# Performance work log

Hardware: AMD Instinct MI355X
Metric: run time of the kernel (lower is better)

Reference implementation:

```python
import jax, jax.numpy as jnp
import numpy as np

INPUT_SIZE = 1024
HIDDEN = 2048
B = 4096


def setup_inputs() -> dict:
    key = jax.random.key(0)
    ks = jax.random.split(key, 11)
    D = INPUT_SIZE + HIDDEN
    bound = 1.0 / np.sqrt(D)  # nn.Linear default init range
    def lin(kw, kb):
        W = jax.random.uniform(kw, (HIDDEN, D), jnp.float32, -bound, bound)
        b = jax.random.uniform(kb, (HIDDEN,), jnp.float32, -bound, bound)
        return W, b
    W_i, b_i = lin(ks[0], ks[1])
    W_f, b_f = lin(ks[2], ks[3])
    W_c, b_c = lin(ks[4], ks[5])
    W_o, b_o = lin(ks[6], ks[7])
    x_t = jax.random.normal(ks[8], (B, INPUT_SIZE), jnp.float32)
    h_prev = jax.random.normal(ks[9], (B, HIDDEN), jnp.float32)
    c_prev = jax.random.normal(ks[10], (B, HIDDEN), jnp.float32)
    return {
        "x_t": x_t, "h_prev": h_prev, "c_prev": c_prev,
        "W_i": W_i, "b_i": b_i, "W_f": W_f, "b_f": b_f,
        "W_c": W_c, "b_c": b_c, "W_o": W_o, "b_o": b_o,
    }


def reference(x_t, h_prev, c_prev, W_i, b_i, W_f, b_f, W_c, b_c, W_o, b_o):
    # combined: [B, input+hidden]
    combined = jnp.concatenate([x_t, h_prev], axis=1)
    # fused gate GEMM: stack the four weight matrices -> one [D, 4H] matmul
    W_all = jnp.concatenate([W_i, W_f, W_c, W_o], axis=0)  # [4H, D]
    b_all = jnp.concatenate([b_i, b_f, b_c, b_o], axis=0)  # [4H]
    gates = combined @ W_all.T + b_all                     # [B, 4H]
    gi, gf, gc, go = jnp.split(gates, 4, axis=1)
    i_t = jax.nn.sigmoid(gi)
    f_t = jax.nn.sigmoid(gf)
    g_t = jnp.tanh(gc)
    o_t = jax.nn.sigmoid(go)
    c_t = f_t * c_prev + i_t * g_t
    h_t = o_t * jnp.tanh(c_t)
    # dropout is identity in eval / p=0
    return (h_t, c_t)
```

## Files before the change

kernel.cpp:

```cpp
#include <hip/hip_runtime.h>
#include <stdint.h>

#define B_DIM 4096
#define IN_SZ 1024
#define HID   2048
#define D_DIM 3072
#define BM 256
#define BN 64
#define BK 64
#define NT (D_DIM / BK)

typedef float  f32x4  __attribute__((ext_vector_type(4)));
typedef short  short8 __attribute__((ext_vector_type(8)));

__device__ __forceinline__ unsigned short f2bf(float f) {
    union { float f; unsigned u; } v; v.f = f;
    unsigned u = v.u + 0x7fffu + ((v.u >> 16) & 1u);
    return (unsigned short)(u >> 16);
}

__device__ __forceinline__ void async_load16(const void* g, void* l) {
    __builtin_amdgcn_global_load_lds(
        (const __attribute__((address_space(1))) unsigned int*)g,
        (__attribute__((address_space(3))) unsigned int*)l,
        16, 0, 0);
}

__device__ __forceinline__ float sigm(float x) {
    return 1.0f / (1.0f + __expf(-x));
}
__device__ __forceinline__ float tanh_f(float x) {
    return 1.0f - 2.0f / (__expf(2.0f * x) + 1.0f);
}

__global__ __launch_bounds__(256)
void convert_all(const float* __restrict__ x, const float* __restrict__ h,
                 const float* __restrict__ W0, const float* __restrict__ W1,
                 const float* __restrict__ W2, const float* __restrict__ W3,
                 unsigned short* __restrict__ Abf, unsigned short* __restrict__ Wbf) {
    const int NA = B_DIM * D_DIM / 8;
    const int NW = 4 * HID * D_DIM / 8;
    int idx = blockIdx.x * blockDim.x + threadIdx.x;
    const float* src;
    unsigned short* dst;
    if (idx < NA) {
        const int C8 = D_DIM / 8;
        int b = idx / C8, c8 = idx - b * C8;
        src = (c8 < IN_SZ / 8) ? x + (size_t)b * IN_SZ + c8 * 8
                               : h + (size_t)b * HID + (c8 - IN_SZ / 8) * 8;
        dst = Abf + (size_t)idx * 8;
    } else {
        int wi = idx - NA;
        if (wi >= NW) return;
        const int PG = HID * D_DIM / 8;
        int g = wi / PG, r = wi - g * PG;
        const float* W = (g == 0) ? W0 : (g == 1) ? W1 : (g == 2) ? W2 : W3;
        src = W + (size_t)r * 8;
        dst = Wbf + (size_t)wi * 8;
    }
    float4 v0 = ((const float4*)src)[0];
    float4 v1 = ((const float4*)src)[1];
    short8 o;
    o[0] = (short)f2bf(v0.x); o[1] = (short)f2bf(v0.y);
    o[2] = (short)f2bf(v0.z); o[3] = (short)f2bf(v0.w);
    o[4] = (short)f2bf(v1.x); o[5] = (short)f2bf(v1.y);
    o[6] = (short)f2bf(v1.z); o[7] = (short)f2bf(v1.w);
    *(short8*)dst = o;
}

template <int IB>
__device__ __forceinline__ void mfma16(f32x4 (&acc)[8][4], const short8 (&a)[4],
                                       const short8 (&b)[4]) {
#pragma unroll
    for (int i = 0; i < 4; ++i)
#pragma unroll
        for (int j = 0; j < 4; ++j)
            acc[IB + i][j] = __builtin_amdgcn_mfma_f32_16x16x32_bf16(
                a[i], b[j], acc[IB + i][j], 0, 0, 0);
}

template <int MODE>
__device__ __forceinline__ void tile_body(
    f32x4 (&acc)[8][4], const char* cur, char* nxt,
    const unsigned short* srcA0, const unsigned short* const* srcB,
    int koff, int chunk, int aBase, int bBase, int sw0, int sw1) {
    const char* curA = cur;
    const char* curB = cur + 32768;
    short8 a0s0[4], a1s0[4], a0s1[4], a1s1[4], bs0[4], bs1[4];

#pragma unroll
    for (int i = 0; i < 4; ++i)
        a0s0[i] = *(const short8*)(curA + aBase + i * 2048 + sw0);
#pragma unroll
    for (int j = 0; j < 4; ++j)
        bs0[j] = *(const short8*)(curB + bBase + j * 2048 + sw0);
#pragma unroll
    for (int i = 0; i < 4; ++i)
        a1s0[i] = *(const short8*)(curA + aBase + (4 + i) * 2048 + sw0);
    if (MODE) {
#pragma unroll
        for (int i = 0; i < 4; ++i)
            async_load16(srcA0 + i * 8 * D_DIM + koff, nxt + chunk + i * 1024);
    }
    __builtin_amdgcn_sched_barrier(0);
    __builtin_amdgcn_s_setprio(1);
    mfma16<0>(acc, a0s0, bs0);
    __builtin_amdgcn_s_setprio(0);

#pragma unroll
    for (int i = 0; i < 4; ++i)
        a0s1[i] = *(const short8*)(curA + aBase + i * 2048 + sw1);
#pragma unroll
    for (int j = 0; j < 4; ++j)
        bs1[j] = *(const short8*)(curB + bBase + j * 2048 + sw1);
    if (MODE) {
#pragma unroll
        for (int i = 0; i < 4; ++i)
            async_load16(srcB[i] + koff, nxt + 32768 + chunk + i * 1024);
    }
    __builtin_amdgcn_sched_barrier(0);
    __builtin_amdgcn_s_setprio(1);
    mfma16<4>(acc, a1s0, bs0);
    __builtin_amdgcn_s_setprio(0);

#pragma unroll
    for (int i = 0; i < 4; ++i)
        a1s1[i] = *(const short8*)(curA + aBase + (4 + i) * 2048 + sw1);
    __builtin_amdgcn_sched_barrier(0);
    __builtin_amdgcn_s_setprio(1);
    mfma16<0>(acc, a0s1, bs1);
    __builtin_amdgcn_s_setprio(0);

    __builtin_amdgcn_sched_barrier(0);
    __builtin_amdgcn_s_setprio(1);
    mfma16<4>(acc, a1s1, bs1);
    __builtin_amdgcn_s_setprio(0);
    if (MODE) {
        asm volatile("s_waitcnt vmcnt(0)" ::: "memory");
        __builtin_amdgcn_s_barrier();
        asm volatile("" ::: "memory");
    }
}

__global__ __launch_bounds__(512, 2)
void lstm_gemm(const unsigned short* __restrict__ Abf,
               const unsigned short* __restrict__ Wbf,
               const float* __restrict__ b_i, const float* __restrict__ b_f,
               const float* __restrict__ b_c, const float* __restrict__ b_o,
               const float* __restrict__ c_prev,
               float* __restrict__ h_out, float* __restrict__ c_out) {
    extern __shared__ char sm[];

    const int tid  = threadIdx.x;
    const int lane = tid & 63;
    const int wave = tid >> 6;
    const int wm   = wave >> 2;
    const int wn   = wave & 3;
    const int l16  = lane & 15;
    const int quad = lane >> 4;
    const int r7   = l16 & 7;

    const int m0 = blockIdx.x * BM;
    const int h0 = blockIdx.y * BN;

    const int g8 = lane >> 3;
    const int sl = (lane & 7) ^ g8;
    const unsigned short* srcA0 = Abf + (size_t)(m0 + wave * 32 + g8) * D_DIM + sl * 8;
    const unsigned short* srcB[4];
#pragma unroll
    for (int i = 0; i < 4; ++i) {
        const int rt = wave * 32 + i * 8 + g8;
        const int grow = ((rt >> 4) & 3) * HID + h0 + (rt >> 6) * 16 + (rt & 15);
        srcB[i] = Wbf + (size_t)grow * D_DIM + sl * 8;
    }
    const int chunk = wave * 4096;

    const int aBase = (wm * 128 + l16) * 128;
    const int bBase = (wn * 64  + l16) * 128;
    const int sw0 = ((0 * 4 + quad) ^ r7) * 16;
    const int sw1 = ((1 * 4 + quad) ^ r7) * 16;

    f32x4 acc[8][4] = {};

#pragma unroll
    for (int i = 0; i < 4; ++i) {
        async_load16(srcB[i], sm + 32768 + chunk + i * 1024);
        async_load16(srcA0 + i * 8 * D_DIM, sm + chunk + i * 1024);
    }
    asm volatile("s_waitcnt vmcnt(0)" ::: "memory");
    __builtin_amdgcn_s_barrier();
    asm volatile("" ::: "memory");

    for (int kt = 0; kt < NT - 1; ++kt) {
        const char* cur = sm + (kt & 1) * 65536;
        char* nxt = (char*)sm + ((kt + 1) & 1) * 65536;
        tile_body<1>(acc, cur, nxt, srcA0, srcB,
                     (kt + 1) * BK, chunk, aBase, bBase, sw0, sw1);
    }
    tile_body<0>(acc, sm + ((NT - 1) & 1) * 65536, (char*)sm,
                 srcA0, srcB, 0, chunk, aBase, bBase, sw0, sw1);

    const int h = h0 + wn * 16 + l16;
    const float biv = b_i[h], bfv = b_f[h], bcv = b_c[h], bov = b_o[h];
    const int mb = m0 + wm * 128 + quad * 4;
#pragma unroll
    for (int i = 0; i < 8; ++i) {
#pragma unroll
        for (int r = 0; r < 4; ++r) {
            const int m = mb + i * 16 + r;
            const size_t off = (size_t)m * HID + h;
            const float gi = acc[i][0][r] + biv;
            const float gf = acc[i][1][r] + bfv;
            const float gc = acc[i][2][r] + bcv;
            const float go = acc[i][3][r] + bov;
            const float it = sigm(gi), ft = sigm(gf);
            const float gt = tanh_f(gc), ot = sigm(go);
            const float c = ft * c_prev[off] + it * gt;
            h_out[off] = ot * tanh_f(c);
            c_out[off] = c;
        }
    }
}

extern "C" void kernel_launch(void* const* d_in, const int* in_sizes, int n_in,
                              void* d_out, int out_size, void* d_ws, size_t ws_size,
                              hipStream_t stream) {
    const float* x_t    = (const float*)d_in[0];
    const float* h_prev = (const float*)d_in[1];
    const float* c_prev = (const float*)d_in[2];
    const float* W_i = (const float*)d_in[3];
    const float* b_i = (const float*)d_in[4];
    const float* W_f = (const float*)d_in[5];
    const float* b_f = (const float*)d_in[6];
    const float* W_c = (const float*)d_in[7];
    const float* b_c = (const float*)d_in[8];
    const float* W_o = (const float*)d_in[9];
    const float* b_o = (const float*)d_in[10];
    float* out = (float*)d_out;

    unsigned short* Abf = (unsigned short*)d_ws;
    unsigned short* Wbf = (unsigned short*)((char*)d_ws + (size_t)B_DIM * D_DIM * 2);

    static bool s_attr = false;
    if (!s_attr) {
        (void)hipFuncSetAttribute((const void*)lstm_gemm,
                                  hipFuncAttributeMaxDynamicSharedMemorySize, 131072);
        s_attr = true;
    }

    {
        const int n = (B_DIM * D_DIM + 4 * HID * D_DIM) / 8;
        convert_all<<<n / 256, 256, 0, stream>>>(x_t, h_prev, W_i, W_f, W_c, W_o,
                                                 Abf, Wbf);
    }
    dim3 grid(B_DIM / BM, HID / BN);
    lstm_gemm<<<grid, 512, 131072, stream>>>(Abf, Wbf, b_i, b_f, b_c, b_o, c_prev,
                                             out, out + (size_t)B_DIM * HID);
}
```

Measured before the change: 383.7 us.

## Prepack weights in MFMA fragment order and load B directly into registers

```diff
diff --git a/kernel.cpp b/kernel.cpp
--- a/kernel.cpp
+++ b/kernel.cpp
@@ -52,10 +52,18 @@
     } else {
         int wi = idx - NA;
         if (wi >= NW) return;
-        const int PG = HID * D_DIM / 8;
-        int g = wi / PG, r = wi - g * PG;
-        const float* W = (g == 0) ? W0 : (g == 1) ? W1 : (g == 2) ? W2 : W3;
-        src = W + (size_t)r * 8;
+        int l  = wi & 63;
+        int q  = wi >> 6;
+        int s  = q & 1;
+        int j  = (q >> 1) & 3;
+        int wn = (q >> 3) & 3;
+        int q3 = q >> 5;
+        int kt = q3 % NT;
+        int c  = q3 / NT;
+        const float* W = (j == 0) ? W0 : (j == 1) ? W1 : (j == 2) ? W2 : W3;
+        int hrow = c * 64 + wn * 16 + (l & 15);
+        int k    = kt * 64 + s * 32 + (l >> 4) * 8;
+        src = W + (size_t)hrow * D_DIM + k;
         dst = Wbf + (size_t)wi * 8;
     }
     float4 v0 = ((const float4*)src)[0];
@@ -68,72 +76,66 @@
     *(short8*)dst = o;
 }
 
-template <int IB>
+template <int IB, int S>
 __device__ __forceinline__ void mfma16(f32x4 (&acc)[8][4], const short8 (&a)[4],
-                                       const short8 (&b)[4]) {
+                                       const short8 (&b)[4][2]) {
 #pragma unroll
     for (int i = 0; i < 4; ++i)
 #pragma unroll
         for (int j = 0; j < 4; ++j)
             acc[IB + i][j] = __builtin_amdgcn_mfma_f32_16x16x32_bf16(
-                a[i], b[j], acc[IB + i][j], 0, 0, 0);
+                a[i], b[j][S], acc[IB + i][j], 0, 0, 0);
 }
 
 template <int MODE>
 __device__ __forceinline__ void tile_body(
-    f32x4 (&acc)[8][4], const char* cur, char* nxt,
-    const unsigned short* srcA0, const unsigned short* const* srcB,
-    int koff, int chunk, int aBase, int bBase, int sw0, int sw1) {
-    const char* curA = cur;
-    const char* curB = cur + 32768;
-    short8 a0s0[4], a1s0[4], a0s1[4], a1s1[4], bs0[4], bs1[4];
-
-#pragma unroll
-    for (int i = 0; i < 4; ++i)
-        a0s0[i] = *(const short8*)(curA + aBase + i * 2048 + sw0);
-#pragma unroll
-    for (int j = 0; j < 4; ++j)
-        bs0[j] = *(const short8*)(curB + bBase + j * 2048 + sw0);
-#pragma unroll
-    for (int i = 0; i < 4; ++i)
-        a1s0[i] = *(const short8*)(curA + aBase + (4 + i) * 2048 + sw0);
+    f32x4 (&acc)[8][4], const short8 (&bc)[4][2], short8 (&bn)[4][2],
+    const char* cur, char* nxt,
+    const unsigned short* pBn,
+    const unsigned short* srcA0,
+    int koff, int chunk, int aBase, int sw0, int sw1) {
+    short8 f1[4], f2[4], f3[4], f4[4];
+
+#pragma unroll
+    for (int i = 0; i < 4; ++i)
+        f1[i] = *(const short8*)(cur + aBase + i * 2048 + sw0);
+#pragma unroll
+    for (int i = 0; i < 4; ++i)
+        f2[i] = *(const short8*)(cur + aBase + (4 + i) * 2048 + sw0);
     if (MODE) {
+#pragma unroll
+        for (int j = 0; j < 4; ++j) {
+            bn[j][0] = *(const short8*)(pBn + (j * 2 + 0) * 512);
+            bn[j][1] = *(const short8*)(pBn + (j * 2 + 1) * 512);
+        }
 #pragma unroll
         for (int i = 0; i < 4; ++i)
             async_load16(srcA0 + i * 8 * D_DIM + koff, nxt + chunk + i * 1024);
     }
     __builtin_amdgcn_sched_barrier(0);
     __builtin_amdgcn_s_setprio(1);
-    mfma16<0>(acc, a0s0, bs0);
-    __builtin_amdgcn_s_setprio(0);
-
-#pragma unroll
-    for (int i = 0; i < 4; ++i)
-        a0s1[i] = *(const short8*)(curA + aBase + i * 2048 + sw1);
-#pragma unroll
-    for (int j = 0; j < 4; ++j)
-        bs1[j] = *(const short8*)(curB + bBase + j * 2048 + sw1);
-    if (MODE) {
-#pragma unroll
-        for (int i = 0; i < 4; ++i)
-            async_load16(srcB[i] + koff, nxt + 32768 + chunk + i * 1024);
-    }
-    __builtin_amdgcn_sched_barrier(0);
-    __builtin_amdgcn_s_setprio(1);
-    mfma16<4>(acc, a1s0, bs0);
-    __builtin_amdgcn_s_setprio(0);
-
-#pragma unroll
-    for (int i = 0; i < 4; ++i)
-        a1s1[i] = *(const short8*)(curA + aBase + (4 + i) * 2048 + sw1);
-    __builtin_amdgcn_sched_barrier(0);
-    __builtin_amdgcn_s_setprio(1);
-    mfma16<0>(acc, a0s1, bs1);
-    __builtin_amdgcn_s_setprio(0);
-
-    __builtin_amdgcn_sched_barrier(0);
-    __builtin_amdgcn_s_setprio(1);
-    mfma16<4>(acc, a1s1, bs1);
+    mfma16<0, 0>(acc, f1, bc);
+    __builtin_amdgcn_s_setprio(0);
+
+#pragma unroll
+    for (int i = 0; i < 4; ++i)
+        f3[i] = *(const short8*)(cur + aBase + i * 2048 + sw1);
+    __builtin_amdgcn_sched_barrier(0);
+    __builtin_amdgcn_s_setprio(1);
+    mfma16<4, 0>(acc, f2, bc);
+    __builtin_amdgcn_s_setprio(0);
+
+#pragma unroll
+    for (int i = 0; i < 4; ++i)
+        f4[i] = *(const short8*)(cur + aBase + (4 + i) * 2048 + sw1);
+    __builtin_amdgcn_sched_barrier(0);
+    __builtin_amdgcn_s_setprio(1);
+    mfma16<0, 1>(acc, f3, bc);
+    __builtin_amdgcn_s_setprio(0);
+
+    __builtin_amdgcn_sched_barrier(0);
+    __builtin_amdgcn_s_setprio(1);
+    mfma16<4, 1>(acc, f4, bc);
     __builtin_amdgcn_s_setprio(0);
     if (MODE) {
         asm volatile("s_waitcnt vmcnt(0)" ::: "memory");
@@ -160,45 +162,57 @@
     const int quad = lane >> 4;
     const int r7   = l16 & 7;
 
-    const int m0 = blockIdx.x * BM;
-    const int h0 = blockIdx.y * BN;
+    const int hwid = blockIdx.x;
+    const int c    = (hwid & 7) + 8 * ((hwid >> 3) & 3);
+    const int bx   = hwid >> 5;
+    const int m0 = bx * BM;
+    const int h0 = c * BN;
 
     const int g8 = lane >> 3;
     const int sl = (lane & 7) ^ g8;
     const unsigned short* srcA0 = Abf + (size_t)(m0 + wave * 32 + g8) * D_DIM + sl * 8;
-    const unsigned short* srcB[4];
-#pragma unroll
-    for (int i = 0; i < 4; ++i) {
-        const int rt = wave * 32 + i * 8 + g8;
-        const int grow = ((rt >> 4) & 3) * HID + h0 + (rt >> 6) * 16 + (rt & 15);
-        srcB[i] = Wbf + (size_t)grow * D_DIM + sl * 8;
-    }
     const int chunk = wave * 4096;
 
+    const unsigned short* pB = Wbf + ((size_t)(c * NT) * 4 + wn) * 4096 + lane * 8;
+
     const int aBase = (wm * 128 + l16) * 128;
-    const int bBase = (wn * 64  + l16) * 128;
     const int sw0 = ((0 * 4 + quad) ^ r7) * 16;
     const int sw1 = ((1 * 4 + quad) ^ r7) * 16;
 
     f32x4 acc[8][4] = {};
-
-#pragma unroll
-    for (int i = 0; i < 4; ++i) {
-        async_load16(srcB[i], sm + 32768 + chunk + i * 1024);
+    short8 b0[4][2], b1[4][2];
+
+#pragma unroll
+    for (int j = 0; j < 4; ++j) {
+        b0[j][0] = *(const short8*)(pB + (j * 2 + 0) * 512);
+        b0[j][1] = *(const short8*)(pB + (j * 2 + 1) * 512);
+    }
+#pragma unroll
+    for (int i = 0; i < 4; ++i)
         async_load16(srcA0 + i * 8 * D_DIM, sm + chunk + i * 1024);
-    }
     asm volatile("s_waitcnt vmcnt(0)" ::: "memory");
     __builtin_amdgcn_s_barrier();
     asm volatile("" ::: "memory");
-
-    for (int kt = 0; kt < NT - 1; ++kt) {
-        const char* cur = sm + (kt & 1) * 65536;
-        char* nxt = (char*)sm + ((kt + 1) & 1) * 65536;
-        tile_body<1>(acc, cur, nxt, srcA0, srcB,
-                     (kt + 1) * BK, chunk, aBase, bBase, sw0, sw1);
-    }
-    tile_body<0>(acc, sm + ((NT - 1) & 1) * 65536, (char*)sm,
-                 srcA0, srcB, 0, chunk, aBase, bBase, sw0, sw1);
+    pB += 16384;
+
+    for (int kt = 0; kt < NT - 2; kt += 2) {
+        const char* e = sm + (kt & 1) * 32768;
+        char*       o = (char*)sm + ((kt + 1) & 1) * 32768;
+        tile_body<1>(acc, b0, b1, e, o, pB, srcA0, (kt + 1) * BK,
+                     chunk, aBase, sw0, sw1);
+        pB += 16384;
+        tile_body<1>(acc, b1, b0, o, (char*)e, pB, srcA0, (kt + 2) * BK,
+                     chunk, aBase, sw0, sw1);
+        pB += 16384;
+    }
+    {
+        tile_body<1>(acc, b0, b1, sm, (char*)sm + 32768, pB, srcA0,
+                     (NT - 1) * BK, chunk, aBase, sw0, sw1);
+    }
+    {
+        tile_body<0>(acc, b1, b0, sm + 32768, (char*)sm, pB, srcA0,
+                     0, chunk, aBase, sw0, sw1);
+    }
 
     const int h = h0 + wn * 16 + l16;
     const float biv = b_i[h], bfv = b_f[h], bcv = b_c[h], bov = b_o[h];
@@ -215,9 +229,9 @@
             const float go = acc[i][3][r] + bov;
             const float it = sigm(gi), ft = sigm(gf);
             const float gt = tanh_f(gc), ot = sigm(go);
-            const float c = ft * c_prev[off] + it * gt;
-            h_out[off] = ot * tanh_f(c);
-            c_out[off] = c;
+            const float cc = ft * c_prev[off] + it * gt;
+            h_out[off] = ot * tanh_f(cc);
+            c_out[off] = cc;
         }
     }
 }
@@ -244,7 +258,7 @@
     static bool s_attr = false;
     if (!s_attr) {
         (void)hipFuncSetAttribute((const void*)lstm_gemm,
-                                  hipFuncAttributeMaxDynamicSharedMemorySize, 131072);
+                                  hipFuncAttributeMaxDynamicSharedMemorySize, 65536);
         s_attr = true;
     }
 
@@ -253,7 +267,6 @@
         convert_all<<<n / 256, 256, 0, stream>>>(x_t, h_prev, W_i, W_f, W_c, W_o,
                                                  Abf, Wbf);
     }
-    dim3 grid(B_DIM / BM, HID / BN);
-    lstm_gemm<<<grid, 512, 131072, stream>>>(Abf, Wbf, b_i, b_f, b_c, b_o, c_prev,
-                                             out, out + (size_t)B_DIM * HID);
-}
+    lstm_gemm<<<512, 512, 65536, stream>>>(Abf, Wbf, b_i, b_f, b_c, b_o, c_prev,
+                                           out, out + (size_t)B_DIM * HID);
+}
```

Measured after the change: 389.9 us. No clear change (+1.6%).

## Use four-stage LDS ring of 32-wide K slices with deeper async prefetch

Applied to the files above, without the earlier changes.

```diff
diff --git a/kernel.cpp b/kernel.cpp
--- a/kernel.cpp
+++ b/kernel.cpp
@@ -7,8 +7,8 @@
 #define D_DIM 3072
 #define BM 256
 #define BN 64
-#define BK 64
-#define NT (D_DIM / BK)
+#define BK2 128
+#define NT2 (D_DIM / BK2)
 
 typedef float  f32x4  __attribute__((ext_vector_type(4)));
 typedef short  short8 __attribute__((ext_vector_type(8)));
@@ -40,32 +40,34 @@
                  unsigned short* __restrict__ Abf, unsigned short* __restrict__ Wbf) {
     const int NA = B_DIM * D_DIM / 8;
     const int NW = 4 * HID * D_DIM / 8;
-    int idx = blockIdx.x * blockDim.x + threadIdx.x;
-    const float* src;
-    unsigned short* dst;
-    if (idx < NA) {
-        const int C8 = D_DIM / 8;
-        int b = idx / C8, c8 = idx - b * C8;
-        src = (c8 < IN_SZ / 8) ? x + (size_t)b * IN_SZ + c8 * 8
-                               : h + (size_t)b * HID + (c8 - IN_SZ / 8) * 8;
-        dst = Abf + (size_t)idx * 8;
-    } else {
-        int wi = idx - NA;
-        if (wi >= NW) return;
-        const int PG = HID * D_DIM / 8;
-        int g = wi / PG, r = wi - g * PG;
-        const float* W = (g == 0) ? W0 : (g == 1) ? W1 : (g == 2) ? W2 : W3;
-        src = W + (size_t)r * 8;
-        dst = Wbf + (size_t)wi * 8;
-    }
-    float4 v0 = ((const float4*)src)[0];
-    float4 v1 = ((const float4*)src)[1];
-    short8 o;
-    o[0] = (short)f2bf(v0.x); o[1] = (short)f2bf(v0.y);
-    o[2] = (short)f2bf(v0.z); o[3] = (short)f2bf(v0.w);
-    o[4] = (short)f2bf(v1.x); o[5] = (short)f2bf(v1.y);
-    o[6] = (short)f2bf(v1.z); o[7] = (short)f2bf(v1.w);
-    *(short8*)dst = o;
+    const int total = NA + NW;
+    for (int idx = blockIdx.x * blockDim.x + threadIdx.x; idx < total;
+         idx += gridDim.x * blockDim.x) {
+        const float* src;
+        unsigned short* dst;
+        if (idx < NA) {
+            const int C8 = D_DIM / 8;
+            int b = idx / C8, c8 = idx - b * C8;
+            src = (c8 < IN_SZ / 8) ? x + (size_t)b * IN_SZ + c8 * 8
+                                   : h + (size_t)b * HID + (c8 - IN_SZ / 8) * 8;
+            dst = Abf + (size_t)idx * 8;
+        } else {
+            int wi = idx - NA;
+            const int PG = HID * D_DIM / 8;
+            int g = wi / PG, r = wi - g * PG;
+            const float* W = (g == 0) ? W0 : (g == 1) ? W1 : (g == 2) ? W2 : W3;
+            src = W + (size_t)r * 8;
+            dst = Wbf + (size_t)wi * 8;
+        }
+        float4 v0 = ((const float4*)src)[0];
+        float4 v1 = ((const float4*)src)[1];
+        short8 o;
+        o[0] = (short)f2bf(v0.x); o[1] = (short)f2bf(v0.y);
+        o[2] = (short)f2bf(v0.z); o[3] = (short)f2bf(v0.w);
+        o[4] = (short)f2bf(v1.x); o[5] = (short)f2bf(v1.y);
+        o[6] = (short)f2bf(v1.z); o[7] = (short)f2bf(v1.w);
+        *(short8*)dst = o;
+    }
 }
 
 template <int IB>
@@ -79,67 +81,36 @@
                 a[i], b[j], acc[IB + i][j], 0, 0, 0);
 }
 
-template <int MODE>
-__device__ __forceinline__ void tile_body(
-    f32x4 (&acc)[8][4], const char* cur, char* nxt,
-    const unsigned short* srcA0, const unsigned short* const* srcB,
-    int koff, int chunk, int aBase, int bBase, int sw0, int sw1) {
-    const char* curA = cur;
-    const char* curB = cur + 32768;
-    short8 a0s0[4], a1s0[4], a0s1[4], a1s1[4], bs0[4], bs1[4];
-
+template <int KS, int SKS>
+__device__ __forceinline__ void pair_body(
+    f32x4 (&acc)[8][4], char* sm, int aOff, int bOff, int wchunk,
+    const unsigned short* sA, const unsigned short* sB0, const unsigned short* sB1,
+    int stElem) {
+    const char* reg = sm + KS * 16384;
+    short8 a0[4], bb[4], a1[4];
 #pragma unroll
     for (int i = 0; i < 4; ++i)
-        a0s0[i] = *(const short8*)(curA + aBase + i * 2048 + sw0);
+        a0[i] = *(const short8*)(reg + aOff + i * 1024);
 #pragma unroll
     for (int j = 0; j < 4; ++j)
-        bs0[j] = *(const short8*)(curB + bBase + j * 2048 + sw0);
+        bb[j] = *(const short8*)(reg + bOff + j * 1024);
 #pragma unroll
     for (int i = 0; i < 4; ++i)
-        a1s0[i] = *(const short8*)(curA + aBase + (4 + i) * 2048 + sw0);
-    if (MODE) {
-#pragma unroll
-        for (int i = 0; i < 4; ++i)
-            async_load16(srcA0 + i * 8 * D_DIM + koff, nxt + chunk + i * 1024);
-    }
+        a1[i] = *(const short8*)(reg + aOff + (4 + i) * 1024);
+    char* dA = sm + SKS * 16384 + wchunk;
+    char* dB = dA + 65536;
+    async_load16(sA + stElem,         dA);
+    async_load16(sA + 49152 + stElem, dA + 1024);
+    async_load16(sB0 + stElem,        dB);
+    async_load16(sB1 + stElem,        dB + 1024);
     __builtin_amdgcn_sched_barrier(0);
     __builtin_amdgcn_s_setprio(1);
-    mfma16<0>(acc, a0s0, bs0);
+    mfma16<0>(acc, a0, bb);
+    mfma16<4>(acc, a1, bb);
     __builtin_amdgcn_s_setprio(0);
-
-#pragma unroll
-    for (int i = 0; i < 4; ++i)
-        a0s1[i] = *(const short8*)(curA + aBase + i * 2048 + sw1);
-#pragma unroll
-    for (int j = 0; j < 4; ++j)
-        bs1[j] = *(const short8*)(curB + bBase + j * 2048 + sw1);
-    if (MODE) {
-#pragma unroll
-        for (int i = 0; i < 4; ++i)
-            async_load16(srcB[i] + koff, nxt + 32768 + chunk + i * 1024);
-    }
-    __builtin_amdgcn_sched_barrier(0);
-    __builtin_amdgcn_s_setprio(1);
-    mfma16<4>(acc, a1s0, bs0);
-    __builtin_amdgcn_s_setprio(0);
-
-#pragma unroll
-    for (int i = 0; i < 4; ++i)
-        a1s1[i] = *(const short8*)(curA + aBase + (4 + i) * 2048 + sw1);
-    __builtin_amdgcn_sched_barrier(0);
-    __builtin_amdgcn_s_setprio(1);
-    mfma16<0>(acc, a0s1, bs1);
-    __builtin_amdgcn_s_setprio(0);
-
-    __builtin_amdgcn_sched_barrier(0);
-    __builtin_amdgcn_s_setprio(1);
-    mfma16<4>(acc, a1s1, bs1);
-    __builtin_amdgcn_s_setprio(0);
-    if (MODE) {
-        asm volatile("s_waitcnt vmcnt(0)" ::: "memory");
-        __builtin_amdgcn_s_barrier();
-        asm volatile("" ::: "memory");
-    }
+    asm volatile("s_waitcnt vmcnt(8)" ::: "memory");
+    __builtin_amdgcn_s_barrier();
+    asm volatile("" ::: "memory");
 }
 
 __global__ __launch_bounds__(512, 2)
@@ -158,47 +129,49 @@
     const int wn   = wave & 3;
     const int l16  = lane & 15;
     const int quad = lane >> 4;
-    const int r7   = l16 & 7;
 
     const int m0 = blockIdx.x * BM;
     const int h0 = blockIdx.y * BN;
 
-    const int g8 = lane >> 3;
-    const int sl = (lane & 7) ^ g8;
-    const unsigned short* srcA0 = Abf + (size_t)(m0 + wave * 32 + g8) * D_DIM + sl * 8;
-    const unsigned short* srcB[4];
-#pragma unroll
-    for (int i = 0; i < 4; ++i) {
-        const int rt = wave * 32 + i * 8 + g8;
-        const int grow = ((rt >> 4) & 3) * HID + h0 + (rt >> 6) * 16 + (rt & 15);
-        srcB[i] = Wbf + (size_t)grow * D_DIM + sl * 8;
-    }
-    const int chunk = wave * 4096;
-
-    const int aBase = (wm * 128 + l16) * 128;
-    const int bBase = (wn * 64  + l16) * 128;
-    const int sw0 = ((0 * 4 + quad) ^ r7) * 16;
-    const int sw1 = ((1 * 4 + quad) ^ r7) * 16;
+    const int srow = lane >> 2;
+    const int sl   = (lane & 3) ^ (srow & 3);
+    const unsigned short* sA = Abf + (size_t)(m0 + wave * 32 + srow) * D_DIM + sl * 8;
+    const int rt0 = wave * 32 + srow;
+    const int rt1 = rt0 + 16;
+    const int g0  = ((rt0 >> 4) & 3) * HID + h0 + (rt0 >> 6) * 16 + (rt0 & 15);
+    const int g1  = ((rt1 >> 4) & 3) * HID + h0 + (rt1 >> 6) * 16 + (rt1 & 15);
+    const unsigned short* sB0 = Wbf + (size_t)g0 * D_DIM + sl * 8;
+    const unsigned short* sB1 = Wbf + (size_t)g1 * D_DIM + sl * 8;
+    const int wchunk = wave * 2048;
+
+    const int slotSw = (quad ^ (l16 & 3)) * 16;
+    const int aOff = (wm * 128 + l16) * 64 + slotSw;
+    const int bOff = 65536 + (wn * 64 + l16) * 64 + slotSw;
 
     f32x4 acc[8][4] = {};
 
 #pragma unroll
-    for (int i = 0; i < 4; ++i) {
-        async_load16(srcB[i], sm + 32768 + chunk + i * 1024);
-        async_load16(srcA0 + i * 8 * D_DIM, sm + chunk + i * 1024);
-    }
-    asm volatile("s_waitcnt vmcnt(0)" ::: "memory");
+    for (int s = 0; s < 3; ++s) {
+        char* dA = sm + s * 16384 + wchunk;
+        char* dB = dA + 65536;
+        const int e = s * 32;
+        async_load16(sA + e,         dA);
+        async_load16(sA + 49152 + e, dA + 1024);
+        async_load16(sB0 + e,        dB);
+        async_load16(sB1 + e,        dB + 1024);
+    }
+    asm volatile("s_waitcnt vmcnt(8)" ::: "memory");
     __builtin_amdgcn_s_barrier();
     asm volatile("" ::: "memory");
 
-    for (int kt = 0; kt < NT - 1; ++kt) {
-        const char* cur = sm + (kt & 1) * 65536;
-        char* nxt = (char*)sm + ((kt + 1) & 1) * 65536;
-        tile_body<1>(acc, cur, nxt, srcA0, srcB,
-                     (kt + 1) * BK, chunk, aBase, bBase, sw0, sw1);
-    }
-    tile_body<0>(acc, sm + ((NT - 1) & 1) * 65536, (char*)sm,
-                 srcA0, srcB, 0, chunk, aBase, bBase, sw0, sw1);
+    for (int kt = 0; kt < NT2; ++kt) {
+        const int kn = (kt < NT2 - 1) ? kt + 1 : kt;
+        pair_body<0, 3>(acc, sm, aOff, bOff, wchunk, sA, sB0, sB1, kt * 128 + 96);
+        pair_body<1, 0>(acc, sm, aOff, bOff, wchunk, sA, sB0, sB1, kn * 128 + 0);
+        pair_body<2, 1>(acc, sm, aOff, bOff, wchunk, sA, sB0, sB1, kn * 128 + 32);
+        pair_body<3, 2>(acc, sm, aOff, bOff, wchunk, sA, sB0, sB1, kn * 128 + 64);
+    }
+    asm volatile("s_waitcnt vmcnt(0)" ::: "memory");
 
     const int h = h0 + wn * 16 + l16;
     const float biv = b_i[h], bfv = b_f[h], bcv = b_c[h], bov = b_o[h];
@@ -215,9 +188,9 @@
             const float go = acc[i][3][r] + bov;
             const float it = sigm(gi), ft = sigm(gf);
             const float gt = tanh_f(gc), ot = sigm(go);
-            const float c = ft * c_prev[off] + it * gt;
-            h_out[off] = ot * tanh_f(c);
-            c_out[off] = c;
+            const float cc = ft * c_prev[off] + it * gt;
+            h_out[off] = ot * tanh_f(cc);
+            c_out[off] = cc;
         }
     }
 }
@@ -248,11 +221,8 @@
         s_attr = true;
     }
 
-    {
-        const int n = (B_DIM * D_DIM + 4 * HID * D_DIM) / 8;
-        convert_all<<<n / 256, 256, 0, stream>>>(x_t, h_prev, W_i, W_f, W_c, W_o,
-                                                 Abf, Wbf);
-    }
+    convert_all<<<2048, 256, 0, stream>>>(x_t, h_prev, W_i, W_f, W_c, W_o, Abf, Wbf);
+
     dim3 grid(B_DIM / BM, HID / BN);
     lstm_gemm<<<grid, 512, 131072, stream>>>(Abf, Wbf, b_i, b_f, b_c, b_o, c_prev,
                                              out, out + (size_t)B_DIM * HID);
```

After: 404.5 us. 1.05x slower.
